# Kernel tuning notes

Measured on AMD Instinct MI355X. Metric: run time of the kernel, lower is better.

## Reference

```python
import jax, jax.numpy as jnp
import numpy as np

NEG_INF = -1000000000.0
EMBED = 1024
HEADS = 16
HEAD_DIM = EMBED // HEADS
BATCH = 2
SEQ = 2048


def setup_inputs() -> dict:
    key = jax.random.key(0)
    ks = jax.random.split(key, 5)
    s = 0.02
    return {
        "x": jax.random.normal(ks[0], (BATCH, SEQ, EMBED), dtype=jnp.float32),
        "W_qkv": jax.random.normal(ks[1], (EMBED, 3 * EMBED), dtype=jnp.float32) * s,
        "b_qkv": jax.random.normal(ks[2], (3 * EMBED,), dtype=jnp.float32) * s,
        "W_out": jax.random.normal(ks[3], (EMBED, EMBED), dtype=jnp.float32) * s,
        "b_out": jax.random.normal(ks[4], (EMBED,), dtype=jnp.float32) * s,
    }


def reference(x, W_qkv, b_qkv, W_out, b_out):
    B, S, E = x.shape
    qkv = x @ W_qkv + b_qkv                      # [B,S,3E]
    qkv = qkv.reshape(B, S, HEADS, 3 * HEAD_DIM).transpose(0, 2, 1, 3)  # [B,H,S,3hd]
    q, k, v = jnp.split(qkv, 3, axis=-1)         # each [B,H,S,hd]
    scale = 1.0 / jnp.sqrt(jnp.float32(HEAD_DIM))
    scores = jnp.einsum("bhqd,bhkd->bhqk", q, k) * scale  # [B,H,S,S]
    # Faithful to source: tril(ones)*NEG_INF masks LOWER triangle incl. diagonal
    mask = jnp.tril(jnp.ones((S, S), dtype=jnp.float32)) * NEG_INF
    scores = scores + mask[None, None, :, :]
    attn = jax.nn.softmax(scores, axis=-1)
    vals = jnp.einsum("bhqk,bhkd->bhqd", attn, v)  # [B,H,S,hd]
    vals = vals.transpose(0, 2, 1, 3).reshape(B, S, E)
    return vals @ W_out + b_out
```

## Files before the change

### kernel.cpp

```cpp
#include <hip/hip_runtime.h>
#include <hip/hip_bf16.h>

#define BATCH 2
#define SEQ 2048
#define EMBED 1024
#define HEADS 16
#define HD 64

typedef __attribute__((ext_vector_type(8))) short short8;
typedef __attribute__((ext_vector_type(4))) float f32x4;
typedef __attribute__((ext_vector_type(16))) float f32x16;
typedef __attribute__((ext_vector_type(4))) int i32x4;
typedef unsigned short u16;

#define C2F 0.18033688f
#define NEGL -1442695040.0f

__device__ __forceinline__ u16 f2bf(float x){
  unsigned u = __builtin_bit_cast(unsigned, x);
  u = (u + 0x7fffu + ((u >> 16) & 1u)) >> 16;
  return (u16)u;
}

__device__ __forceinline__ float fexp2(float x){
  float r;
  asm("v_exp_f32 %0, %1" : "=v"(r) : "v"(x));
  return r;
}

__device__ __forceinline__ void gload16(const u16* g, u16* l){
  __builtin_amdgcn_global_load_lds(
      (const __attribute__((address_space(1))) unsigned int*)g,
      (__attribute__((address_space(3))) unsigned int*)l, 16, 0, 0);
}

__global__ void k_cvt(const float* __restrict__ in, u16* __restrict__ out){
  int i = blockIdx.x * blockDim.x + threadIdx.x;
  float4 v = reinterpret_cast<const float4*>(in)[i];
  ushort4 o;
  o.x = f2bf(v.x); o.y = f2bf(v.y); o.z = f2bf(v.z); o.w = f2bf(v.w);
  reinterpret_cast<ushort4*>(out)[i] = o;
}

__global__ void k_transpose(const float* __restrict__ in, u16* __restrict__ out,
                            int K, int N){
  __shared__ float tile[32][33];
  int n0 = blockIdx.x * 32, k0 = blockIdx.y * 32;
  int tx = threadIdx.x, ty = threadIdx.y;
  #pragma unroll
  for (int i = 0; i < 32; i += 8)
    tile[ty + i][tx] = in[(size_t)(k0 + ty + i) * N + n0 + tx];
  __syncthreads();
  #pragma unroll
  for (int i = 0; i < 32; i += 8)
    out[(size_t)(n0 + ty + i) * K + k0 + tx] = f2bf(tile[tx][ty + i]);
}

__global__ __launch_bounds__(256) void k_gemm_qkv(
    const u16* __restrict__ A, const u16* __restrict__ Bt,
    const float* __restrict__ bias,
    u16* __restrict__ qb, u16* __restrict__ kbf, u16* __restrict__ vt)
{
  const int K = 1024;
  __shared__ __align__(16) u16 sbuf[128*144];
  u16* As = sbuf;
  u16* Bs = sbuf + 4096;
  int t = threadIdx.x;
  int wave = t >> 6, lane = t & 63;
  int g = lane >> 4, c = lane & 15;
  int wr = wave >> 1, wc = wave & 1;
  int mb = blockIdx.y * 128, nb = blockIdx.x * 128;

  const u16* ga = A  + (size_t)(mb + wave*32 + (lane>>2)) * K + (lane&3)*8;
  const u16* gb = Bt + (size_t)(nb + wave*32 + (lane>>2)) * K + (lane&3)*8;
  u16* la = &As[wave*1024];
  u16* lb = &Bs[wave*1024];

  f32x4 acc[4][4] = {};
  for (int k = 0; k < K; k += 32){
    gload16(ga + k,          la);
    gload16(ga + k + 16*K,   la + 512);
    gload16(gb + k,          lb);
    gload16(gb + k + 16*K,   lb + 512);
    __syncthreads();
    short8 af[4], bf[4];
    #pragma unroll
    for (int i = 0; i < 4; i++){
      af[i] = *reinterpret_cast<const short8*>(&As[(wr*64 + i*16 + c)*32 + 8*g]);
      bf[i] = *reinterpret_cast<const short8*>(&Bs[(wc*64 + i*16 + c)*32 + 8*g]);
    }
    #pragma unroll
    for (int i = 0; i < 4; i++)
      #pragma unroll
      for (int j = 0; j < 4; j++)
        acc[i][j] = __builtin_amdgcn_mfma_f32_16x16x32_bf16(af[i], bf[j], acc[i][j], 0, 0, 0);
    __syncthreads();
  }

  u16 (*Cs)[144] = (u16(*)[144])sbuf;
  #pragma unroll
  for (int i = 0; i < 4; i++)
  #pragma unroll
  for (int j = 0; j < 4; j++)
  #pragma unroll
  for (int r = 0; r < 4; r++){
    int row = wr*64 + i*16 + 4*g + r;
    int col = wc*64 + j*16 + c;
    int gcol = nb + col;
    float vv = acc[i][j][r] + bias[gcol];
    if ((gcol % 192) < 64) vv *= C2F;
    Cs[row][col] = f2bf(vv);
  }
  __syncthreads();

  int b  = mb >> 11;
  int sb = mb & 2047;
  for (int cell = wave; cell < 32; cell += 4){
    int s32 = cell >> 3;
    int cg  = cell & 7;
    int col0 = nb + cg*16;
    int h   = col0 / 192;
    int rem = col0 - h*192;
    int sel = rem >> 6;
    int d0  = rem & 63;
    size_t hb = (size_t)(b * HEADS + h);
    if (sel < 2){
      int sl  = lane & 31;
      int dhi = lane >> 5;
      int s   = sb + s32*32 + sl;
      size_t off = (((hb*64 + (size_t)(s>>5))*4 + (size_t)(d0>>4))*64 + (size_t)lane)*8;
      const short8 v = *reinterpret_cast<const short8*>(&Cs[s32*32 + sl][cg*16 + dhi*8]);
      u16* dst = (sel == 0 ? qb : kbf) + off;
      *reinterpret_cast<short8*>(dst) = v;
    } else {
      int dl   = lane & 15;
      int soct = lane >> 4;
      int d    = d0 + dl;
      int sl0  = s32*32 + soct*8;
      int s0   = sb + sl0;
      int lanep = (d & 31) | (((s0 >> 3) & 1) << 5);
      size_t off = (((hb*128 + (size_t)(s0>>4))*2 + (size_t)(d>>5))*64 + (size_t)lanep)*8;
      u16 tmp[8];
      #pragma unroll
      for (int k2 = 0; k2 < 8; k2++) tmp[k2] = Cs[sl0 + k2][cg*16 + dl];
      *reinterpret_cast<short8*>(vt + off) = *reinterpret_cast<const short8*>(tmp);
    }
  }
}

template<int B>
__device__ __forceinline__ short8 pack_pa(const f32x16& p){
  unsigned X, Y, Z, W;
  asm("v_cvt_pk_bf16_f32 %0, %1, %2" : "=v"(X) : "v"(p[B+0]), "v"(p[B+1]));
  asm("v_cvt_pk_bf16_f32 %0, %1, %2" : "=v"(Y) : "v"(p[B+2]), "v"(p[B+3]));
  asm("v_cvt_pk_bf16_f32 %0, %1, %2" : "=v"(Z) : "v"(p[B+4]), "v"(p[B+5]));
  asm("v_cvt_pk_bf16_f32 %0, %1, %2" : "=v"(W) : "v"(p[B+6]), "v"(p[B+7]));
  asm("v_permlane32_swap_b32 %0, %1" : "+v"(X), "+v"(Z));
  asm("v_permlane32_swap_b32 %0, %1" : "+v"(Y), "+v"(W));
  i32x4 w = { (int)X, (int)Y, (int)Z, (int)W };
  return __builtin_bit_cast(short8, w);
}

__global__ __launch_bounds__(256) void k_attn(
    const u16* __restrict__ qb, const u16* __restrict__ kbuf,
    const u16* __restrict__ vt, u16* __restrict__ vals)
{
  __shared__ __align__(16) u16 po[4][32][72];
  __shared__ float pmv[4][32];
  __shared__ float plv[4][32];

  int wave = threadIdx.x >> 6, lane = threadIdx.x & 63;
  int hi = lane >> 5, ln = lane & 31;
  int d0 = blockIdx.x;
  int x   = d0 & 7;
  int kk  = d0 >> 3;
  int grp = kk >> 6;
  int qr  = kk & 63;
  int qidx = (qr == 0) ? 63 : qr - 1;
  int bh  = x + 8 * grp;
  int qw  = qidx * 32;
  int qg  = qw + ln;

  const u16* Qf = qb   + (size_t)bh*131072 + ((size_t)(qw>>5)*4)*512 + (size_t)lane*8;
  const u16* Kf = kbuf + (size_t)bh*131072 + (size_t)lane*8;
  const u16* Vf = vt   + (size_t)bh*131072 + (size_t)lane*8;

  short8 qf[4];
  #pragma unroll
  for (int kc = 0; kc < 4; kc++)
    qf[kc] = *reinterpret_cast<const short8*>(Qf + (size_t)kc*512);

  f32x16 o0 = {}, o1 = {};
  float m, l_part = 0.f;

  if (qidx < 63){
    m = 0.f;
    int kb_first = qw + wave*32;
    short8 kfc[4];
    if (kb_first < SEQ){
      int tk = (kb_first >> 5) * 4;
      #pragma unroll
      for (int kc = 0; kc < 4; kc++)
        kfc[kc] = *reinterpret_cast<const short8*>(Kf + (size_t)(tk + kc)*512);
    }
    for (int kb = kb_first; kb < SEQ; kb += 128){
      int tv = (kb >> 4) * 2;
      short8 vf0 = *reinterpret_cast<const short8*>(Vf + (size_t)(tv + 0)*512);
      short8 vf1 = *reinterpret_cast<const short8*>(Vf + (size_t)(tv + 1)*512);
      short8 vf2 = *reinterpret_cast<const short8*>(Vf + (size_t)(tv + 2)*512);
      short8 vf3 = *reinterpret_cast<const short8*>(Vf + (size_t)(tv + 3)*512);
      int kbn = kb + 128;
      int tkn = ((kbn < SEQ ? kbn : kb) >> 5) * 4;
      short8 kfn[4];
      #pragma unroll
      for (int kc = 0; kc < 4; kc++)
        kfn[kc] = *reinterpret_cast<const short8*>(Kf + (size_t)(tkn + kc)*512);
      f32x16 s0 = {};
      __builtin_amdgcn_s_setprio(1);
      #pragma unroll
      for (int kc = 0; kc < 4; kc++)
        s0 = __builtin_amdgcn_mfma_f32_32x32x16_bf16(kfc[kc], qf[kc], s0, 0, 0, 0);
      __builtin_amdgcn_s_setprio(0);
      if (kb <= qw + 31){
        #pragma unroll
        for (int r = 0; r < 16; r++){
          int kv = kb + 4*hi + (r & 3) + 8*(r >> 2);
          s0[r] += (kv <= qg) ? NEGL : 0.f;
        }
      }
      float ps = 0.f;
      #pragma unroll
      for (int r = 0; r < 16; r++){
        s0[r] = fexp2(s0[r]);
        ps += s0[r];
      }
      l_part += ps;
      short8 pa0 = pack_pa<0>(s0), pa1 = pack_pa<8>(s0);
      __builtin_amdgcn_s_setprio(1);
      o0 = __builtin_amdgcn_mfma_f32_32x32x16_bf16(pa0, vf0, o0, 0, 0, 0);
      o1 = __builtin_amdgcn_mfma_f32_32x32x16_bf16(pa0, vf1, o1, 0, 0, 0);
      o0 = __builtin_amdgcn_mfma_f32_32x32x16_bf16(pa1, vf2, o0, 0, 0, 0);
      o1 = __builtin_amdgcn_mfma_f32_32x32x16_bf16(pa1, vf3, o1, 0, 0, 0);
      __builtin_amdgcn_s_setprio(0);
      #pragma unroll
      for (int kc = 0; kc < 4; kc++) kfc[kc] = kfn[kc];
    }
  } else {
    m = -INFINITY;
    int kb_first = wave*32;
    short8 kfc[4];
    {
      int tk = (kb_first >> 5) * 4;
      #pragma unroll
      for (int kc = 0; kc < 4; kc++)
        kfc[kc] = *reinterpret_cast<const short8*>(Kf + (size_t)(tk + kc)*512);
    }
    for (int kb = kb_first; kb < SEQ; kb += 128){
      int tv = (kb >> 4) * 2;
      short8 vf0 = *reinterpret_cast<const short8*>(Vf + (size_t)(tv + 0)*512);
      short8 vf1 = *reinterpret_cast<const short8*>(Vf + (size_t)(tv + 1)*512);
      short8 vf2 = *reinterpret_cast<const short8*>(Vf + (size_t)(tv + 2)*512);
      short8 vf3 = *reinterpret_cast<const short8*>(Vf + (size_t)(tv + 3)*512);
      int kbn = kb + 128;
      int tkn = ((kbn < SEQ ? kbn : kb) >> 5) * 4;
      short8 kfn[4];
      #pragma unroll
      for (int kc = 0; kc < 4; kc++)
        kfn[kc] = *reinterpret_cast<const short8*>(Kf + (size_t)(tkn + kc)*512);
      f32x16 s0 = {};
      __builtin_amdgcn_s_setprio(1);
      #pragma unroll
      for (int kc = 0; kc < 4; kc++)
        s0 = __builtin_amdgcn_mfma_f32_32x32x16_bf16(kfc[kc], qf[kc], s0, 0, 0, 0);
      __builtin_amdgcn_s_setprio(0);
      #pragma unroll
      for (int r = 0; r < 16; r++){
        int kv = kb + 4*hi + (r & 3) + 8*(r >> 2);
        s0[r] += (kv <= qg) ? NEGL : 0.f;
      }
      float t0 = fmaxf(fmaxf(s0[0], s0[4]), fmaxf(s0[8],  s0[12]));
      float t1 = fmaxf(fmaxf(s0[1], s0[5]), fmaxf(s0[9],  s0[13]));
      float t2 = fmaxf(fmaxf(s0[2], s0[6]), fmaxf(s0[10], s0[14]));
      float t3 = fmaxf(fmaxf(s0[3], s0[7]), fmaxf(s0[11], s0[15]));
      float pmx = fmaxf(fmaxf(t0, t1), fmaxf(t2, t3));
      if (__any(pmx > m + 8.0f)){
        float pmf = fmaxf(pmx, __shfl_xor(pmx, 32));
        float mn = fmaxf(m, pmf);
        float al = fexp2(m - mn);
        #pragma unroll
        for (int r = 0; r < 16; r++){
          float alr = __shfl(al, (r & 3) + 8*(r >> 2) + 4*hi);
          o0[r] *= alr; o1[r] *= alr;
        }
        l_part *= al;
        m = mn;
      }
      float negm = -m;
      float ps = 0.f;
      #pragma unroll
      for (int r = 0; r < 16; r++){
        s0[r] = fexp2(s0[r] + negm);
        ps += s0[r];
      }
      l_part += ps;
      short8 pa0 = pack_pa<0>(s0), pa1 = pack_pa<8>(s0);
      __builtin_amdgcn_s_setprio(1);
      o0 = __builtin_amdgcn_mfma_f32_32x32x16_bf16(pa0, vf0, o0, 0, 0, 0);
      o1 = __builtin_amdgcn_mfma_f32_32x32x16_bf16(pa0, vf1, o1, 0, 0, 0);
      o0 = __builtin_amdgcn_mfma_f32_32x32x16_bf16(pa1, vf2, o0, 0, 0, 0);
      o1 = __builtin_amdgcn_mfma_f32_32x32x16_bf16(pa1, vf3, o1, 0, 0, 0);
      __builtin_amdgcn_s_setprio(0);
      #pragma unroll
      for (int kc = 0; kc < 4; kc++) kfc[kc] = kfn[kc];
    }
  }

  float l = l_part + __shfl_xor(l_part, 32);

  #pragma unroll
  for (int r = 0; r < 16; r++){
    int row = (r & 3) + 8*(r >> 2) + 4*hi;
    po[wave][row][ln]      = f2bf(o0[r]);
    po[wave][row][32 + ln] = f2bf(o1[r]);
  }
  if (hi == 0){ pmv[wave][ln] = m; plv[wave][ln] = l; }
  __syncthreads();

  int t   = threadIdx.x;
  int row = t >> 3;
  int c8  = (t & 7) * 8;
  float m0 = pmv[0][row], m1 = pmv[1][row], m2 = pmv[2][row], m3 = pmv[3][row];
  float ms = fmaxf(fmaxf(m0, m1), fmaxf(m2, m3));
  float f0 = fexp2(m0 - ms), f1 = fexp2(m1 - ms);
  float f2 = fexp2(m2 - ms), f3 = fexp2(m3 - ms);
  float ls = plv[0][row]*f0 + plv[1][row]*f1 + plv[2][row]*f2 + plv[3][row]*f3;
  float inv = 1.0f / ls;
  f0 *= inv; f1 *= inv; f2 *= inv; f3 *= inv;
  int b = bh >> 4, h = bh & 15;
  u16 tmp[8];
  #pragma unroll
  for (int i = 0; i < 8; i += 4){
    ushort4 w0 = *reinterpret_cast<const ushort4*>(&po[0][row][c8 + i]);
    ushort4 w1 = *reinterpret_cast<const ushort4*>(&po[1][row][c8 + i]);
    ushort4 w2 = *reinterpret_cast<const ushort4*>(&po[2][row][c8 + i]);
    ushort4 w3 = *reinterpret_cast<const ushort4*>(&po[3][row][c8 + i]);
    const u16* p0 = (const u16*)&w0; const u16* p1 = (const u16*)&w1;
    const u16* p2 = (const u16*)&w2; const u16* p3 = (const u16*)&w3;
    #pragma unroll
    for (int j = 0; j < 4; j++){
      float v = __builtin_bit_cast(float, (unsigned)p0[j] << 16) * f0
              + __builtin_bit_cast(float, (unsigned)p1[j] << 16) * f1
              + __builtin_bit_cast(float, (unsigned)p2[j] << 16) * f2
              + __builtin_bit_cast(float, (unsigned)p3[j] << 16) * f3;
      tmp[i + j] = f2bf(v);
    }
  }
  u16* dst = vals + ((size_t)(b * SEQ + qw + row)) * EMBED + h * HD + c8;
  *reinterpret_cast<ushort4*>(dst)     = *reinterpret_cast<ushort4*>(&tmp[0]);
  *reinterpret_cast<ushort4*>(dst + 4) = *reinterpret_cast<ushort4*>(&tmp[4]);
}

__global__ __launch_bounds__(256) void k_gemm_out(
    const u16* __restrict__ A, const u16* __restrict__ Bt,
    const float* __restrict__ bias, float* __restrict__ out)
{
  const int K = 1024;
  __shared__ __align__(16) u16 As[64*32];
  __shared__ __align__(16) u16 Bs[128*32];
  int t = threadIdx.x;
  int wave = t >> 6, lane = t & 63;
  int g = lane >> 4, c = lane & 15;
  int wr = wave >> 1, wc = wave & 1;
  int mb = blockIdx.y * 64, nb = blockIdx.x * 128;

  const u16* ga = A  + (size_t)(mb + wave*16 + (lane>>2)) * K + (lane&3)*8;
  const u16* gb = Bt + (size_t)(nb + wave*32 + (lane>>2)) * K + (lane&3)*8;
  u16* la = &As[wave*512];
  u16* lb = &Bs[wave*1024];

  f32x4 acc[2][4] = {};
  for (int k = 0; k < K; k += 32){
    gload16(ga + k,          la);
    gload16(gb + k,          lb);
    gload16(gb + k + 16*K,   lb + 512);
    __syncthreads();
    short8 af[2], bf[4];
    #pragma unroll
    for (int i = 0; i < 2; i++)
      af[i] = *reinterpret_cast<const short8*>(&As[(wr*32 + i*16 + c)*32 + 8*g]);
    #pragma unroll
    for (int j = 0; j < 4; j++)
      bf[j] = *reinterpret_cast<const short8*>(&Bs[(wc*64 + j*16 + c)*32 + 8*g]);
    #pragma unroll
    for (int i = 0; i < 2; i++)
      #pragma unroll
      for (int j = 0; j < 4; j++)
        acc[i][j] = __builtin_amdgcn_mfma_f32_16x16x32_bf16(af[i], bf[j], acc[i][j], 0, 0, 0);
    __syncthreads();
  }

  #pragma unroll
  for (int i = 0; i < 2; i++)
  #pragma unroll
  for (int j = 0; j < 4; j++)
  #pragma unroll
  for (int r = 0; r < 4; r++){
    int row = mb + wr*32 + i*16 + 4*g + r;
    int col = nb + wc*64 + j*16 + c;
    out[(size_t)row * EMBED + col] = acc[i][j][r] + bias[col];
  }
}

extern "C" void kernel_launch(void* const* d_in, const int* in_sizes, int n_in,
                              void* d_out, int out_size, void* d_ws, size_t ws_size,
                              hipStream_t stream){
  const float* x    = (const float*)d_in[0];
  const float* Wqkv = (const float*)d_in[1];
  const float* bqkv = (const float*)d_in[2];
  const float* Wout = (const float*)d_in[3];
  const float* bout = (const float*)d_in[4];
  float* out = (float*)d_out;

  char* ws = (char*)d_ws;
  u16* x_bf   = (u16*)(ws);
  u16* wqkv_t = (u16*)(ws + ( 8u << 20));
  u16* wout_t = (u16*)(ws + (14u << 20));
  u16* qbuf   = (u16*)(ws + (16u << 20));
  u16* kbuf   = (u16*)(ws + (24u << 20));
  u16* vtbuf  = (u16*)(ws + (32u << 20));
  u16* vals   = (u16*)(ws + (40u << 20));

  k_cvt<<<4096, 256, 0, stream>>>(x, x_bf);
  dim3 tb(32, 8);
  k_transpose<<<dim3(3072/32, 1024/32), tb, 0, stream>>>(Wqkv, wqkv_t, 1024, 3072);
  k_transpose<<<dim3(1024/32, 1024/32), tb, 0, stream>>>(Wout, wout_t, 1024, 1024);
  k_gemm_qkv<<<dim3(3072/128, 4096/128), 256, 0, stream>>>(x_bf, wqkv_t, bqkv, qbuf, kbuf, vtbuf);
  k_attn<<<2048, 256, 0, stream>>>(qbuf, kbuf, vtbuf, vals);
  k_gemm_out<<<dim3(1024/128, 4096/64), 256, 0, stream>>>(vals, wout_t, bout, out);
}
```

Measured before the change: 109.8 us.

## Software-pipeline QK^T MFMA one block ahead of softmax and PV in causal loop

The main attention loop for non-final query tiles now computes the score MFMAs for the next key block before doing the exp/mask/PV work on the current block, ping-ponging two score accumulators. K fragments are prefetched two blocks ahead. This is meant to overlap MFMA latency with the exp2 VALU work and hide load latency. It costs an extra 16-float accumulator of registers, which may lower occupancy or cause spills.

```diff
diff --git a/kernel.cpp b/kernel.cpp
--- a/kernel.cpp
+++ b/kernel.cpp
@@ -196,54 +196,72 @@
   if (qidx < 63){
     m = 0.f;
     int kb_first = qw + wave*32;
-    short8 kfc[4];
     if (kb_first < SEQ){
-      int tk = (kb_first >> 5) * 4;
+      short8 kA[4];
+      {
+        int tk = (kb_first >> 5) * 4;
+        #pragma unroll
+        for (int kc = 0; kc < 4; kc++)
+          kA[kc] = *reinterpret_cast<const short8*>(Kf + (size_t)(tk + kc)*512);
+      }
+      f32x16 s_a = {}, s_b;
+      __builtin_amdgcn_s_setprio(1);
       #pragma unroll
       for (int kc = 0; kc < 4; kc++)
-        kfc[kc] = *reinterpret_cast<const short8*>(Kf + (size_t)(tk + kc)*512);
-    }
-    for (int kb = kb_first; kb < SEQ; kb += 128){
-      int tv = (kb >> 4) * 2;
-      short8 vf0 = *reinterpret_cast<const short8*>(Vf + (size_t)(tv + 0)*512);
-      short8 vf1 = *reinterpret_cast<const short8*>(Vf + (size_t)(tv + 1)*512);
-      short8 vf2 = *reinterpret_cast<const short8*>(Vf + (size_t)(tv + 2)*512);
-      short8 vf3 = *reinterpret_cast<const short8*>(Vf + (size_t)(tv + 3)*512);
-      int kbn = kb + 128;
-      int tkn = ((kbn < SEQ ? kbn : kb) >> 5) * 4;
-      short8 kfn[4];
-      #pragma unroll
-      for (int kc = 0; kc < 4; kc++)
-        kfn[kc] = *reinterpret_cast<const short8*>(Kf + (size_t)(tkn + kc)*512);
-      f32x16 s0 = {};
-      __builtin_amdgcn_s_setprio(1);
-      #pragma unroll
-      for (int kc = 0; kc < 4; kc++)
-        s0 = __builtin_amdgcn_mfma_f32_32x32x16_bf16(kfc[kc], qf[kc], s0, 0, 0, 0);
+        s_a = __builtin_amdgcn_mfma_f32_32x32x16_bf16(kA[kc], qf[kc], s_a, 0, 0, 0);
       __builtin_amdgcn_s_setprio(0);
-      if (kb <= qw + 31){
+      {
+        int kb2 = kb_first + 128;
+        int tk2 = ((kb2 < SEQ ? kb2 : kb_first) >> 5) * 4;
+        #pragma unroll
+        for (int kc = 0; kc < 4; kc++)
+          kA[kc] = *reinterpret_cast<const short8*>(Kf + (size_t)(tk2 + kc)*512);
+      }
+      auto step = [&](f32x16& scur, f32x16& snxt, int KB){
+        int tv = (KB >> 4) * 2;
+        short8 vf0 = *reinterpret_cast<const short8*>(Vf + (size_t)(tv + 0)*512);
+        short8 vf1 = *reinterpret_cast<const short8*>(Vf + (size_t)(tv + 1)*512);
+        short8 vf2 = *reinterpret_cast<const short8*>(Vf + (size_t)(tv + 2)*512);
+        short8 vf3 = *reinterpret_cast<const short8*>(Vf + (size_t)(tv + 3)*512);
+        f32x16 z = {};
+        __builtin_amdgcn_s_setprio(1);
+        #pragma unroll
+        for (int kc = 0; kc < 4; kc++)
+          z = __builtin_amdgcn_mfma_f32_32x32x16_bf16(kA[kc], qf[kc], z, 0, 0, 0);
+        __builtin_amdgcn_s_setprio(0);
+        snxt = z;
+        int kbn = KB + 256;
+        int tkn = ((kbn < SEQ ? kbn : KB) >> 5) * 4;
+        #pragma unroll
+        for (int kc = 0; kc < 4; kc++)
+          kA[kc] = *reinterpret_cast<const short8*>(Kf + (size_t)(tkn + kc)*512);
+        if (KB <= qw + 31){
+          #pragma unroll
+          for (int r = 0; r < 16; r++){
+            int kv = KB + 4*hi + (r & 3) + 8*(r >> 2);
+            scur[r] += (kv <= qg) ? NEGL : 0.f;
+          }
+        }
+        float ps = 0.f;
         #pragma unroll
         for (int r = 0; r < 16; r++){
-          int kv = kb + 4*hi + (r & 3) + 8*(r >> 2);
-          s0[r] += (kv <= qg) ? NEGL : 0.f;
+          scur[r] = fexp2(scur[r]);
+          ps += scur[r];
         }
-      }
-      float ps = 0.f;
-      #pragma unroll
-      for (int r = 0; r < 16; r++){
-        s0[r] = fexp2(s0[r]);
-        ps += s0[r];
-      }
-      l_part += ps;
-      short8 pa0 = pack_pa<0>(s0), pa1 = pack_pa<8>(s0);
-      __builtin_amdgcn_s_setprio(1);
-      o0 = __builtin_amdgcn_mfma_f32_32x32x16_bf16(pa0, vf0, o0, 0, 0, 0);
-      o1 = __builtin_amdgcn_mfma_f32_32x32x16_bf16(pa0, vf1, o1, 0, 0, 0);
-      o0 = __builtin_amdgcn_mfma_f32_32x32x16_bf16(pa1, vf2, o0, 0, 0, 0);
-      o1 = __builtin_amdgcn_mfma_f32_32x32x16_bf16(pa1, vf3, o1, 0, 0, 0);
-      __builtin_amdgcn_s_setprio(0);
-      #pragma unroll
-      for (int kc = 0; kc < 4; kc++) kfc[kc] = kfn[kc];
+        l_part += ps;
+        short8 pa0 = pack_pa<0>(scur), pa1 = pack_pa<8>(scur);
+        __builtin_amdgcn_s_setprio(1);
+        o0 = __builtin_amdgcn_mfma_f32_32x32x16_bf16(pa0, vf0, o0, 0, 0, 0);
+        o1 = __builtin_amdgcn_mfma_f32_32x32x16_bf16(pa0, vf1, o1, 0, 0, 0);
+        o0 = __builtin_amdgcn_mfma_f32_32x32x16_bf16(pa1, vf2, o0, 0, 0, 0);
+        o1 = __builtin_amdgcn_mfma_f32_32x32x16_bf16(pa1, vf3, o1, 0, 0, 0);
+        __builtin_amdgcn_s_setprio(0);
+      };
+      int kb = kb_first;
+      for (;;){
+        step(s_a, s_b, kb); kb += 128; if (kb >= SEQ) break;
+        step(s_b, s_a, kb); kb += 128; if (kb >= SEQ) break;
+      }
     }
   } else {
     m = -INFINITY;
```

New measurement: 111.2 us. Within noise of the previous version (+1.3%).
